# Optimization experiments

Measured on AMD Instinct MI355X. Metric: run time of the kernel, lower is better.

## Reference

```python
import jax, jax.numpy as jnp
import numpy as np

N_NODES = 100000
N_EDGES = 1600000
IN_CH = 128
HID = 128
OUT_CH = 16
N_GRAPHS = 64


def setup_inputs() -> dict:
    key = jax.random.key(0)
    ks = jax.random.split(key, 8)
    x = jax.random.normal(ks[0], (N_NODES, IN_CH), dtype=jnp.float32)
    edge_index = jax.random.randint(ks[1], (2, N_EDGES), 0, N_NODES, dtype=jnp.int64)
    batch = jnp.sort(jax.random.randint(ks[2], (N_NODES,), 0, N_GRAPHS, dtype=jnp.int64))
    s1 = 1.0 / np.sqrt(IN_CH)
    s2 = 1.0 / np.sqrt(HID)
    W1 = jax.random.uniform(ks[3], (IN_CH, HID), jnp.float32, -s1, s1)
    b1 = jnp.zeros((HID,), jnp.float32)
    W2 = jax.random.uniform(ks[4], (HID, HID), jnp.float32, -s2, s2)
    b2 = jnp.zeros((HID,), jnp.float32)
    Wfc = jax.random.uniform(ks[5], (HID, OUT_CH), jnp.float32, -s2, s2)
    bfc = jax.random.uniform(ks[6], (OUT_CH,), jnp.float32, -s2, s2)
    return {"x": x, "W1": W1, "b1": b1, "W2": W2, "b2": b2,
            "Wfc": Wfc, "bfc": bfc, "edge_index": edge_index, "batch": batch}


def _gcn_conv(x, W, b, src, dst, deg_inv_sqrt, deg_inv):
    # GCNConv with self-loops: out = D^-1/2 (A+I) D^-1/2 (x W) + b
    h = x @ W                                   # [N, H]
    norm = deg_inv_sqrt[src] * deg_inv_sqrt[dst]  # [E]
    agg = jax.ops.segment_sum(h[src] * norm[:, None], dst, num_segments=N_NODES)
    # self-loop term: deg_inv_sqrt[i]^2 * h[i]
    return agg + h * deg_inv[:, None] + b


def reference(x, W1, b1, W2, b2, Wfc, bfc, edge_index, batch):
    src, dst = edge_index[0], edge_index[1]
    # degree including self-loop
    deg = jax.ops.segment_sum(jnp.ones((N_EDGES,), jnp.float32), dst, num_segments=N_NODES) + 1.0
    deg_inv_sqrt = jax.lax.rsqrt(deg)
    deg_inv = 1.0 / deg
    h = jax.nn.relu(_gcn_conv(x, W1, b1, src, dst, deg_inv_sqrt, deg_inv))
    h = jax.nn.relu(_gcn_conv(h, W2, b2, src, dst, deg_inv_sqrt, deg_inv))
    # global mean pool over graphs
    sums = jax.ops.segment_sum(h, batch, num_segments=N_GRAPHS)          # [G, H]
    counts = jax.ops.segment_sum(jnp.ones((N_NODES,), jnp.float32), batch, num_segments=N_GRAPHS)
    pooled = sums / jnp.maximum(counts, 1.0)[:, None]
    return pooled @ Wfc + bfc
```

## Files before the change

### kernel.cpp

```cpp
#include <hip/hip_runtime.h>
#include <math.h>

#define NN 100000
#define NE 1600000
#define CH 128
#define OUTC 16
#define NG 64

#define CBSH 9
#define NCB 196
#define CHK 8192
#define MAXB 12288
#define PS 8
#define LDA 136

#define GEMMB 782
#define HISTB 196
#define PREPB 391

typedef __attribute__((ext_vector_type(8))) short bf16x8;
typedef __attribute__((ext_vector_type(4))) float f32x4;

__device__ __forceinline__ unsigned short f2bf(float f) {
    union { float f; unsigned u; } v; v.f = f;
    unsigned r = v.u + 0x7FFF + ((v.u >> 16) & 1);
    return (unsigned short)(r >> 16);
}
__device__ __forceinline__ float bflo(unsigned u) {
    union { unsigned u; float f; } v; v.u = u << 16; return v.f;
}
__device__ __forceinline__ float bfhi(unsigned u) {
    union { unsigned u; float f; } v; v.u = u & 0xffff0000u; return v.f;
}

__launch_bounds__(256, 2)
__global__ void k_fused0(const float* __restrict__ x, const float* __restrict__ W1,
                         const float* __restrict__ W2,
                         unsigned short* __restrict__ wt2,
                         const int* __restrict__ batch, int* __restrict__ gptr,
                         int* __restrict__ gfill, float* __restrict__ pooled,
                         const int* __restrict__ edst, int* __restrict__ hpart,
                         unsigned short* __restrict__ bufA) {
    __shared__ unsigned short wlds[128 * LDA];
    int b = blockIdx.x;
    int t = threadIdx.x;

    if (b < GEMMB) {
#pragma unroll
        for (int it = 0; it < 64; it++) {
            int i = it * 256 + t;
            int k = i >> 7, n = i & 127;
            wlds[n * LDA + k] = f2bf(W1[i]);
        }
        __syncthreads();

        int wave = t >> 6, lane = t & 63;
        int quad = lane >> 4, l16 = lane & 15;
        int rbase = b * 128 + wave * 32;

        bf16x8 af[2][4];
#pragma unroll
        for (int s = 0; s < 2; s++) {
            int row = rbase + s * 16 + l16;
            if (row >= NN) row = NN - 1;
            const float* arow = x + (size_t)row * CH + quad * 8;
#pragma unroll
            for (int ks = 0; ks < 4; ks++) {
                float4 lo = *(const float4*)(arow + ks * 32);
                float4 hi = *(const float4*)(arow + ks * 32 + 4);
                union { bf16x8 v; unsigned short u[8]; } tmp;
                tmp.u[0] = f2bf(lo.x); tmp.u[1] = f2bf(lo.y);
                tmp.u[2] = f2bf(lo.z); tmp.u[3] = f2bf(lo.w);
                tmp.u[4] = f2bf(hi.x); tmp.u[5] = f2bf(hi.y);
                tmp.u[6] = f2bf(hi.z); tmp.u[7] = f2bf(hi.w);
                af[s][ks] = tmp.v;
            }
        }

        f32x4 acc[2][8];
#pragma unroll
        for (int s = 0; s < 2; s++)
#pragma unroll
            for (int tt = 0; tt < 8; tt++) acc[s][tt] = (f32x4){0.f, 0.f, 0.f, 0.f};

#pragma unroll
        for (int tt = 0; tt < 8; tt++) {
            const unsigned short* wcol = &wlds[(tt * 16 + l16) * LDA + quad * 8];
            bf16x8 b0 = *(const bf16x8*)(wcol);
            bf16x8 b1 = *(const bf16x8*)(wcol + 32);
            bf16x8 b2 = *(const bf16x8*)(wcol + 64);
            bf16x8 b3 = *(const bf16x8*)(wcol + 96);
#pragma unroll
            for (int s = 0; s < 2; s++) {
                acc[s][tt] = __builtin_amdgcn_mfma_f32_16x16x32_bf16(af[s][0], b0, acc[s][tt], 0, 0, 0);
                acc[s][tt] = __builtin_amdgcn_mfma_f32_16x16x32_bf16(af[s][1], b1, acc[s][tt], 0, 0, 0);
                acc[s][tt] = __builtin_amdgcn_mfma_f32_16x16x32_bf16(af[s][2], b2, acc[s][tt], 0, 0, 0);
                acc[s][tt] = __builtin_amdgcn_mfma_f32_16x16x32_bf16(af[s][3], b3, acc[s][tt], 0, 0, 0);
            }
        }

#pragma unroll
        for (int s = 0; s < 2; s++) {
#pragma unroll
            for (int r = 0; r < 4; r++) {
                int orow = rbase + s * 16 + quad * 4 + r;
                if (orow < NN) {
#pragma unroll
                    for (int tt = 0; tt < 8; tt++)
                        bufA[(size_t)orow * CH + tt * 16 + l16] = f2bf(acc[s][tt][r]);
                }
            }
        }
    } else if (b < GEMMB + HISTB) {
        int* h = (int*)wlds;
        if (t < NCB) h[t] = 0;
        __syncthreads();
        int hb = b - GEMMB;
        int base = hb * CHK;
#pragma unroll
        for (int i = 0; i < 32; i++) {
            int e = base + i * 256 + t;
            if (e < NE) atomicAdd(&h[edst[e] >> CBSH], 1);
        }
        __syncthreads();
        if (t < NCB) hpart[hb * NCB + t] = h[t];
    } else {
        int i = (b - GEMMB - HISTB) * 256 + t;
        if (i < CH * CH) {
            int k = i >> 7, n = i & 127;
            wt2[n * CH + k] = f2bf(W2[i]);
        }
        if (i < NCB) gfill[i] = 0;
        if (i < NG * CH) pooled[i] = 0.f;
        if (i < NN) {
            int bb = batch[i];
            int prev = (i == 0) ? -1 : batch[i - 1];
            for (int g = prev + 1; g <= bb; g++) gptr[g] = i;
            if (i == NN - 1) {
                for (int g = bb + 1; g <= NG; g++) gptr[g] = NN;
            }
        }
    }
}

__global__ __launch_bounds__(256) void k_bscan(const int* __restrict__ hpart,
                                               int* __restrict__ ebase) {
    __shared__ int s[256];
    int t = threadIdx.x;
    int sum = 0;
    if (t < NCB)
        for (int b = 0; b < HISTB; b++) sum += hpart[b * NCB + t];
    s[t] = (t < NCB) ? sum : 0;
    __syncthreads();
    for (int off = 1; off < 256; off <<= 1) {
        int v = 0;
        if (t >= off) v = s[t - off];
        __syncthreads();
        s[t] += v;
        __syncthreads();
    }
    if (t == 0) ebase[0] = 0;
    if (t < NCB) ebase[t + 1] = s[t];
}

__global__ __launch_bounds__(1024) void k_passA(const int* __restrict__ src, const int* __restrict__ dst,
                        const int* __restrict__ ebase, int* __restrict__ gfill,
                        unsigned* __restrict__ ebuf) {
    __shared__ unsigned lbuf[CHK];
    __shared__ unsigned char lbyte[CHK];
    __shared__ int hcnt[NCB];
    __shared__ int hbase[256];
    __shared__ int goff[NCB];
    int t = threadIdx.x;
    if (t < NCB) hcnt[t] = 0;
    __syncthreads();
    int base = blockIdx.x * CHK;
    int cb[8], slot[8]; unsigned pk[8];
#pragma unroll
    for (int i = 0; i < 8; i++) {
        int e = base + i * 1024 + t;
        cb[i] = -1;
        if (e < NE) {
            int d = dst[e], s = src[e];
            cb[i] = d >> CBSH;
            pk[i] = ((unsigned)s << CBSH) | (unsigned)(d & 511);
            slot[i] = atomicAdd(&hcnt[cb[i]], 1);
        }
    }
    __syncthreads();
    if (t < 256) hbase[t] = (t < NCB) ? hcnt[t] : 0;
    __syncthreads();
    for (int off = 1; off < 256; off <<= 1) {
        int v = 0;
        if (t < 256 && t >= off) v = hbase[t - off];
        __syncthreads();
        if (t < 256) hbase[t] += v;
        __syncthreads();
    }
    if (t < NCB) {
        int c = hcnt[t];
        int g = c ? atomicAdd(&gfill[t], c) : 0;
        goff[t] = ebase[t] + g - (hbase[t] - c);
    }
    __syncthreads();
#pragma unroll
    for (int i = 0; i < 8; i++) {
        if (cb[i] >= 0) {
            int pos = hbase[cb[i]] - hcnt[cb[i]] + slot[i];
            lbuf[pos] = pk[i];
            lbyte[pos] = (unsigned char)cb[i];
        }
    }
    __syncthreads();
    int total = min(NE - base, CHK);
    for (int p = t; p < total; p += 1024) {
        unsigned v = lbuf[p];
        int b = lbyte[p];
        ebuf[goff[b] + p] = v;
    }
}

__global__ __launch_bounds__(1024) void k_passB(const unsigned* __restrict__ ebuf, const int* __restrict__ ebase,
                        int* __restrict__ degi, int* __restrict__ rowst,
                        float* __restrict__ dis, int* __restrict__ csr) {
    __shared__ int cnt[512];
    __shared__ int nbase[512];
    __shared__ int fill[512];
    __shared__ int stage[MAXB];
    int t = threadIdx.x;
    int cb = blockIdx.x;
    int nb0 = cb << CBSH;
    int ncnt = min(512, NN - nb0);
    int e0 = ebase[cb], e1 = ebase[cb + 1];
    if (t < 512) { cnt[t] = 0; fill[t] = 0; }
    __syncthreads();
    for (int e = e0 + t; e < e1; e += 1024)
        atomicAdd(&cnt[ebuf[e] & 511], 1);
    __syncthreads();
    if (t < 512) nbase[t] = cnt[t];
    __syncthreads();
    for (int off = 1; off < 512; off <<= 1) {
        int v = 0;
        if (t < 512 && t >= off) v = nbase[t - off];
        __syncthreads();
        if (t < 512) nbase[t] += v;
        __syncthreads();
    }
    for (int e = e0 + t; e < e1; e += 1024) {
        unsigned v = ebuf[e];
        int local = v & 511;
        int s = atomicAdd(&fill[local], 1);
        stage[nbase[local] - cnt[local] + s] = (int)(v >> CBSH);
    }
    __syncthreads();
    int total = e1 - e0;
    for (int p = t; p < total; p += 1024) csr[e0 + p] = stage[p];
    if (t < ncnt) {
        int c = cnt[t];
        degi[nb0 + t] = c;
        rowst[nb0 + t] = e0 + nbase[t] - c;
        dis[nb0 + t] = rsqrtf((float)c + 1.0f);
    }
}

__global__ __launch_bounds__(256) void k_agg_w(const unsigned short* __restrict__ ht, const int* __restrict__ rowst,
                      const int* __restrict__ degi, const int* __restrict__ csr,
                      const float* __restrict__ dis, const float* __restrict__ bias,
                      unsigned short* __restrict__ out) {
    int t = threadIdx.x;
    int grp = t >> 4;
    int q = t & 15;
    int n = blockIdx.x * 16 + grp;
    const uint4* base = (const uint4*)ht;

    float d = dis[n];
    uint4 sv = base[(size_t)n * 16 + q];
    float a[8];
    a[0] = d * bflo(sv.x); a[1] = d * bfhi(sv.x);
    a[2] = d * bflo(sv.y); a[3] = d * bfhi(sv.y);
    a[4] = d * bflo(sv.z); a[5] = d * bfhi(sv.z);
    a[6] = d * bflo(sv.w); a[7] = d * bfhi(sv.w);

    int start = rowst[n];
    int c = degi[n];
    int nb = c & ~7;
    int j = 0;
    for (; j < nb; j += 8) {
        int idx[8];
#pragma unroll
        for (int u = 0; u < 8; u++) idx[u] = csr[start + j + u];
        uint4 v[8]; float w[8];
#pragma unroll
        for (int u = 0; u < 8; u++) v[u] = base[(size_t)idx[u] * 16 + q];
#pragma unroll
        for (int u = 0; u < 8; u++) w[u] = dis[idx[u]];
#pragma unroll
        for (int u = 0; u < 8; u++) {
            a[0] = fmaf(w[u], bflo(v[u].x), a[0]); a[1] = fmaf(w[u], bfhi(v[u].x), a[1]);
            a[2] = fmaf(w[u], bflo(v[u].y), a[2]); a[3] = fmaf(w[u], bfhi(v[u].y), a[3]);
            a[4] = fmaf(w[u], bflo(v[u].z), a[4]); a[5] = fmaf(w[u], bfhi(v[u].z), a[5]);
            a[6] = fmaf(w[u], bflo(v[u].w), a[6]); a[7] = fmaf(w[u], bfhi(v[u].w), a[7]);
        }
    }
    if (j < c) {
        int idx[8];
#pragma unroll
        for (int u = 0; u < 8; u++) { int e = j + u; idx[u] = csr[start + (e < c ? e : c - 1)]; }
        uint4 v[8]; float w[8];
#pragma unroll
        for (int u = 0; u < 8; u++) v[u] = base[(size_t)idx[u] * 16 + q];
#pragma unroll
        for (int u = 0; u < 8; u++) w[u] = dis[idx[u]];
#pragma unroll
        for (int u = 0; u < 8; u++) {
            if (j + u < c) {
                a[0] = fmaf(w[u], bflo(v[u].x), a[0]); a[1] = fmaf(w[u], bfhi(v[u].x), a[1]);
                a[2] = fmaf(w[u], bflo(v[u].y), a[2]); a[3] = fmaf(w[u], bfhi(v[u].y), a[3]);
                a[4] = fmaf(w[u], bflo(v[u].z), a[4]); a[5] = fmaf(w[u], bfhi(v[u].z), a[5]);
                a[6] = fmaf(w[u], bflo(v[u].w), a[6]); a[7] = fmaf(w[u], bfhi(v[u].w), a[7]);
            }
        }
    }

    const float4* bp = (const float4*)bias;
    float4 b0 = bp[q * 2], b1 = bp[q * 2 + 1];
    uint4 o;
    {
        float ox = fmaxf(fmaf(d, a[0], b0.x), 0.f), oy = fmaxf(fmaf(d, a[1], b0.y), 0.f);
        o.x = ((unsigned)f2bf(oy) << 16) | (unsigned)f2bf(ox);
        ox = fmaxf(fmaf(d, a[2], b0.z), 0.f); oy = fmaxf(fmaf(d, a[3], b0.w), 0.f);
        o.y = ((unsigned)f2bf(oy) << 16) | (unsigned)f2bf(ox);
        ox = fmaxf(fmaf(d, a[4], b1.x), 0.f); oy = fmaxf(fmaf(d, a[5], b1.y), 0.f);
        o.z = ((unsigned)f2bf(oy) << 16) | (unsigned)f2bf(ox);
        ox = fmaxf(fmaf(d, a[6], b1.z), 0.f); oy = fmaxf(fmaf(d, a[7], b1.w), 0.f);
        o.w = ((unsigned)f2bf(oy) << 16) | (unsigned)f2bf(ox);
    }
    ((uint4*)out)[(size_t)n * 16 + q] = o;
}

__launch_bounds__(256, 2)
__global__ void k_gemm2(const unsigned short* __restrict__ Av,
                        const unsigned short* __restrict__ WT,
                        const float* __restrict__ dis,
                        unsigned short* __restrict__ out) {
    int tid = threadIdx.x;
    int wave = tid >> 6, lane = tid & 63;
    int quad = lane >> 4, l16 = lane & 15;

    int rbase = blockIdx.x * 128 + wave * 32;

    bf16x8 af[2][4];
#pragma unroll
    for (int s = 0; s < 2; s++) {
        int row = rbase + s * 16 + l16;
        if (row >= NN) row = NN - 1;
        const unsigned short* arow = Av + (size_t)row * CH + quad * 8;
#pragma unroll
        for (int ks = 0; ks < 4; ks++) af[s][ks] = *(const bf16x8*)(arow + ks * 32);
    }

    f32x4 acc[2][8];
#pragma unroll
    for (int s = 0; s < 2; s++)
#pragma unroll
        for (int t = 0; t < 8; t++) acc[s][t] = (f32x4){0.f, 0.f, 0.f, 0.f};

#pragma unroll
    for (int t = 0; t < 8; t++) {
        const unsigned short* wcol = WT + (size_t)(t * 16 + l16) * CH + quad * 8;
        bf16x8 b0 = *(const bf16x8*)(wcol);
        bf16x8 b1 = *(const bf16x8*)(wcol + 32);
        bf16x8 b2 = *(const bf16x8*)(wcol + 64);
        bf16x8 b3 = *(const bf16x8*)(wcol + 96);
#pragma unroll
        for (int s = 0; s < 2; s++) {
            acc[s][t] = __builtin_amdgcn_mfma_f32_16x16x32_bf16(af[s][0], b0, acc[s][t], 0, 0, 0);
            acc[s][t] = __builtin_amdgcn_mfma_f32_16x16x32_bf16(af[s][1], b1, acc[s][t], 0, 0, 0);
            acc[s][t] = __builtin_amdgcn_mfma_f32_16x16x32_bf16(af[s][2], b2, acc[s][t], 0, 0, 0);
            acc[s][t] = __builtin_amdgcn_mfma_f32_16x16x32_bf16(af[s][3], b3, acc[s][t], 0, 0, 0);
        }
    }

#pragma unroll
    for (int s = 0; s < 2; s++) {
#pragma unroll
        for (int r = 0; r < 4; r++) {
            int orow = rbase + s * 16 + quad * 4 + r;
            if (orow < NN) {
                float d = dis[orow];
#pragma unroll
                for (int t = 0; t < 8; t++) {
                    out[(size_t)orow * CH + t * 16 + l16] = f2bf(acc[s][t][r] * d);
                }
            }
        }
    }
}

__global__ __launch_bounds__(256) void k_agg(const unsigned short* __restrict__ ht, const int* __restrict__ rowst,
                      const int* __restrict__ degi, const int* __restrict__ csr,
                      const float* __restrict__ dis, const float* __restrict__ bias,
                      unsigned short* __restrict__ out) {
    int t = threadIdx.x;
    int grp = t >> 4;
    int q = t & 15;
    int n = blockIdx.x * 16 + grp;
    const uint4* base = (const uint4*)ht;

    uint4 sv = base[(size_t)n * 16 + q];
    float a[8];
    a[0] = bflo(sv.x); a[1] = bfhi(sv.x);
    a[2] = bflo(sv.y); a[3] = bfhi(sv.y);
    a[4] = bflo(sv.z); a[5] = bfhi(sv.z);
    a[6] = bflo(sv.w); a[7] = bfhi(sv.w);

    int start = rowst[n];
    int c = degi[n];
    int nb = c & ~7;
    int j = 0;
    for (; j < nb; j += 8) {
        int idx[8];
#pragma unroll
        for (int u = 0; u < 8; u++) idx[u] = csr[start + j + u];
        uint4 v[8];
#pragma unroll
        for (int u = 0; u < 8; u++) v[u] = base[(size_t)idx[u] * 16 + q];
#pragma unroll
        for (int u = 0; u < 8; u++) {
            a[0] += bflo(v[u].x); a[1] += bfhi(v[u].x);
            a[2] += bflo(v[u].y); a[3] += bfhi(v[u].y);
            a[4] += bflo(v[u].z); a[5] += bfhi(v[u].z);
            a[6] += bflo(v[u].w); a[7] += bfhi(v[u].w);
        }
    }
    if (j < c) {
        int idx[8];
#pragma unroll
        for (int u = 0; u < 8; u++) { int e = j + u; idx[u] = csr[start + (e < c ? e : c - 1)]; }
        uint4 v[8];
#pragma unroll
        for (int u = 0; u < 8; u++) v[u] = base[(size_t)idx[u] * 16 + q];
#pragma unroll
        for (int u = 0; u < 8; u++) {
            if (j + u < c) {
                a[0] += bflo(v[u].x); a[1] += bfhi(v[u].x);
                a[2] += bflo(v[u].y); a[3] += bfhi(v[u].y);
                a[4] += bflo(v[u].z); a[5] += bfhi(v[u].z);
                a[6] += bflo(v[u].w); a[7] += bfhi(v[u].w);
            }
        }
    }

    float d = dis[n];
    const float4* bp = (const float4*)bias;
    float4 b0 = bp[q * 2], b1 = bp[q * 2 + 1];
    uint4 o;
    {
        float ox = fmaxf(fmaf(d, a[0], b0.x), 0.f), oy = fmaxf(fmaf(d, a[1], b0.y), 0.f);
        o.x = ((unsigned)f2bf(oy) << 16) | (unsigned)f2bf(ox);
        ox = fmaxf(fmaf(d, a[2], b0.z), 0.f); oy = fmaxf(fmaf(d, a[3], b0.w), 0.f);
        o.y = ((unsigned)f2bf(oy) << 16) | (unsigned)f2bf(ox);
        ox = fmaxf(fmaf(d, a[4], b1.x), 0.f); oy = fmaxf(fmaf(d, a[5], b1.y), 0.f);
        o.z = ((unsigned)f2bf(oy) << 16) | (unsigned)f2bf(ox);
        ox = fmaxf(fmaf(d, a[6], b1.z), 0.f); oy = fmaxf(fmaf(d, a[7], b1.w), 0.f);
        o.w = ((unsigned)f2bf(oy) << 16) | (unsigned)f2bf(ox);
    }
    ((uint4*)out)[(size_t)n * 16 + q] = o;
}

__global__ __launch_bounds__(512) void k_pool2(const unsigned short* __restrict__ h,
                                               const int* __restrict__ gptr,
                                               float* __restrict__ pooled) {
    int g = blockIdx.x >> 3;
    int s = blockIdx.x & 7;
    int gs = gptr[g], ge = gptr[g + 1];
    int len = ge - gs;
    int i0 = gs + (int)(((long long)len * s) >> 3);
    int i1 = gs + (int)(((long long)len * (s + 1)) >> 3);
    int t = threadIdx.x;
    int pr = t & 63;
    int ro = t >> 6;
    const unsigned* base = (const unsigned*)h;
    float s0 = 0.f, s1 = 0.f;
    for (int n = i0 + ro; n < i1; n += 8) {
        unsigned v = base[(size_t)n * 64 + pr];
        s0 += bflo(v); s1 += bfhi(v);
    }
    __shared__ float red[2][8][64];
    red[0][ro][pr] = s0; red[1][ro][pr] = s1;
    __syncthreads();
    for (int off = 4; off >= 1; off >>= 1) {
        if (ro < off) {
            red[0][ro][pr] += red[0][ro + off][pr];
            red[1][ro][pr] += red[1][ro + off][pr];
        }
        __syncthreads();
    }
    if (ro == 0) {
        atomicAdd(&pooled[g * CH + pr * 2],     red[0][0][pr]);
        atomicAdd(&pooled[g * CH + pr * 2 + 1], red[1][0][pr]);
    }
}

__global__ void k_final(const float* __restrict__ pooled, const int* __restrict__ gptr,
                        const float* __restrict__ Wfc, const float* __restrict__ bfc,
                        float* __restrict__ out) {
    int idx = blockIdx.x * 256 + threadIdx.x;
    if (idx >= NG * OUTC) return;
    int g = idx >> 4, o = idx & 15;
    float c = (float)(gptr[g + 1] - gptr[g]);
    float inv = 1.0f / fmaxf(c, 1.0f);
    float s = 0.f;
    for (int k = 0; k < CH; k++) s += pooled[g * CH + k] * Wfc[k * OUTC + o];
    out[idx] = fmaf(s, inv, bfc[o]);
}

extern "C" void kernel_launch(void* const* d_in, const int* in_sizes, int n_in,
                              void* d_out, int out_size, void* d_ws, size_t ws_size,
                              hipStream_t stream) {
    (void)in_sizes; (void)n_in; (void)out_size; (void)ws_size;
    const float* x   = (const float*)d_in[0];
    const float* W1  = (const float*)d_in[1];
    const float* b1  = (const float*)d_in[2];
    const float* W2  = (const float*)d_in[3];
    const float* b2  = (const float*)d_in[4];
    const float* Wfc = (const float*)d_in[5];
    const float* bfc = (const float*)d_in[6];
    const int* ei    = (const int*)d_in[7];
    const int* batch = (const int*)d_in[8];
    const int* esrc = ei;
    const int* edst = ei + NE;
    float* out = (float*)d_out;

    char* w = (char*)d_ws;
    unsigned short* bufA = (unsigned short*)w; w += (size_t)NN * CH * 2;
    unsigned short* bufB = (unsigned short*)w; w += (size_t)NN * CH * 2;
    unsigned short* wt2  = (unsigned short*)w; w += (size_t)CH * CH * 2;
    unsigned* ebuf = (unsigned*)w; w += (size_t)NE * 4;
    int* csr    = (int*)w;    w += (size_t)NE * 4;
    int* degi   = (int*)w;    w += (size_t)NN * 4;
    int* rowst  = (int*)w;    w += (size_t)NN * 4;
    float* dis  = (float*)w;  w += (size_t)NN * 4;
    int* hpart  = (int*)w;    w += (size_t)HISTB * NCB * 4;
    int* ebase  = (int*)w;    w += (NCB + 1) * 4;
    int* gfill  = (int*)w;    w += NCB * 4;
    int* gptr   = (int*)w;    w += (NG + 1) * 4;
    float* pooled = (float*)w; w += (size_t)NG * CH * 4;

    const int fusedBlocks = GEMMB + HISTB + PREPB;
    const int gemmBlocks = (NN + 127) / 128;
    const int aggBlocks  = NN / 16;

    k_fused0<<<fusedBlocks, 256, 0, stream>>>(x, W1, W2, wt2, batch, gptr, gfill,
                                              pooled, edst, hpart, bufA);
    k_bscan<<<1, 256, 0, stream>>>(hpart, ebase);
    k_passA<<<HISTB, 1024, 0, stream>>>(esrc, edst, ebase, gfill, ebuf);
    k_passB<<<NCB, 1024, 0, stream>>>(ebuf, ebase, degi, rowst, dis, csr);

    k_agg_w<<<aggBlocks, 256, 0, stream>>>(bufA, rowst, degi, csr, dis, b1, bufB);
    k_gemm2<<<gemmBlocks, 256, 0, stream>>>(bufB, wt2, dis, bufA);
    k_agg<<<aggBlocks, 256, 0, stream>>>(bufA, rowst, degi, csr, dis, b2, bufB);

    k_pool2<<<NG * PS, 512, 0, stream>>>(bufB, gptr, pooled);
    k_final<<<(NG * OUTC + 255) / 256, 256, 0, stream>>>(pooled, gptr, Wfc, bfc, out);
}
```

Measured before the change: 313.7 us.

## Restructure CSR build: finer buckets, fuse scan into passA, co-schedule GEMM1 with passB

Halves the destination bucket width (256 nodes, 391 buckets) and removes the separate bucket-scan kernel. The histogram is now reduced with global atomics into a single count array, and every passA block redoes the exclusive scan itself. The first-layer GEMM moves from the early fused kernel into a new kernel alongside the per-bucket CSR finalisation, so the two overlap, and passA uses 512-thread blocks. This removes one launch and the serial hpart reduction, at the cost of redundant scans, a memset, global atomics, and LDS usage that can limit occupancy.

New measurement: 312.9 us (median of 2 runs). About the same (-0.3%).

```diff
diff --git a/kernel.cpp b/kernel.cpp
--- a/kernel.cpp
+++ b/kernel.cpp
@@ -7,16 +7,15 @@
 #define OUTC 16
 #define NG 64
 
-#define CBSH 9
-#define NCB 196
-#define CHK 8192
-#define MAXB 12288
+#define CBSH 8
+#define NCB 391
+#define CHK 4096
+#define HCHK 8192
+#define HISTB 196
+#define PREPB 391
+#define MAXB 6144
 #define PS 8
 #define LDA 136
-
-#define GEMMB 782
-#define HISTB 196
-#define PREPB 391
 
 typedef __attribute__((ext_vector_type(8))) short bf16x8;
 typedef __attribute__((ext_vector_type(4))) float f32x4;
@@ -33,19 +32,158 @@
     union { unsigned u; float f; } v; v.u = u & 0xffff0000u; return v.f;
 }
 
-__launch_bounds__(256, 2)
-__global__ void k_fused0(const float* __restrict__ x, const float* __restrict__ W1,
-                         const float* __restrict__ W2,
-                         unsigned short* __restrict__ wt2,
+__global__ __launch_bounds__(256) void k_fused0(const int* __restrict__ edst, int* __restrict__ bcnt,
+                         const float* __restrict__ W2, unsigned short* __restrict__ wt2,
                          const int* __restrict__ batch, int* __restrict__ gptr,
-                         int* __restrict__ gfill, float* __restrict__ pooled,
-                         const int* __restrict__ edst, int* __restrict__ hpart,
-                         unsigned short* __restrict__ bufA) {
-    __shared__ unsigned short wlds[128 * LDA];
+                         int* __restrict__ gfill, float* __restrict__ pooled) {
     int b = blockIdx.x;
     int t = threadIdx.x;
-
-    if (b < GEMMB) {
+    if (b < HISTB) {
+        __shared__ int h[NCB];
+        for (int i = t; i < NCB; i += 256) h[i] = 0;
+        __syncthreads();
+        int base = b * HCHK;
+#pragma unroll
+        for (int i = 0; i < 32; i++) {
+            int e = base + i * 256 + t;
+            if (e < NE) atomicAdd(&h[edst[e] >> CBSH], 1);
+        }
+        __syncthreads();
+        for (int i = t; i < NCB; i += 256)
+            if (h[i]) atomicAdd(&bcnt[i], h[i]);
+    } else {
+        int i = (b - HISTB) * 256 + t;
+        if (i < CH * CH) {
+            int k = i >> 7, n = i & 127;
+            wt2[n * CH + k] = f2bf(W2[i]);
+        }
+        if (i < NCB) gfill[i] = 0;
+        if (i < NG * CH) pooled[i] = 0.f;
+        if (i < NN) {
+            int bb = batch[i];
+            int prev = (i == 0) ? -1 : batch[i - 1];
+            for (int g = prev + 1; g <= bb; g++) gptr[g] = i;
+            if (i == NN - 1) {
+                for (int g = bb + 1; g <= NG; g++) gptr[g] = NN;
+            }
+        }
+    }
+}
+
+__global__ __launch_bounds__(512) void k_passA(const int* __restrict__ src, const int* __restrict__ dst,
+                        const int* __restrict__ bcnt, int* __restrict__ gfill,
+                        unsigned* __restrict__ ebuf, int* __restrict__ ebase) {
+    __shared__ unsigned lbuf[CHK];
+    __shared__ unsigned short lbkt[CHK];
+    __shared__ int hcnt[NCB];
+    __shared__ int hbase[512];
+    __shared__ int eb[512];
+    __shared__ int goff[NCB];
+    int t = threadIdx.x;
+    for (int i = t; i < NCB; i += 512) hcnt[i] = 0;
+    eb[t] = (t < NCB) ? bcnt[t] : 0;
+    __syncthreads();
+    int base = blockIdx.x * CHK;
+    int cb[8], slot[8]; unsigned pk[8];
+#pragma unroll
+    for (int i = 0; i < 8; i++) {
+        int e = base + i * 512 + t;
+        cb[i] = -1;
+        if (e < NE) {
+            int d = dst[e], s = src[e];
+            cb[i] = d >> CBSH;
+            pk[i] = ((unsigned)s << CBSH) | (unsigned)(d & 255);
+            slot[i] = atomicAdd(&hcnt[cb[i]], 1);
+        }
+    }
+    __syncthreads();
+    hbase[t] = (t < NCB) ? hcnt[t] : 0;
+    __syncthreads();
+    for (int off = 1; off < 512; off <<= 1) {
+        int v1 = 0, v2 = 0;
+        if (t >= off) { v1 = hbase[t - off]; v2 = eb[t - off]; }
+        __syncthreads();
+        if (t >= off) { hbase[t] += v1; eb[t] += v2; }
+        __syncthreads();
+    }
+    if (t < NCB) {
+        int c = hcnt[t];
+        int g = c ? atomicAdd(&gfill[t], c) : 0;
+        int eb_ex = t ? eb[t - 1] : 0;
+        goff[t] = eb_ex + g - (hbase[t] - c);
+    }
+    if (blockIdx.x == 0) {
+        if (t == 0) ebase[0] = 0;
+        if (t < NCB) ebase[t + 1] = eb[t];
+    }
+    __syncthreads();
+#pragma unroll
+    for (int i = 0; i < 8; i++) {
+        if (cb[i] >= 0) {
+            int pos = hbase[cb[i]] - hcnt[cb[i]] + slot[i];
+            lbuf[pos] = pk[i];
+            lbkt[pos] = (unsigned short)cb[i];
+        }
+    }
+    __syncthreads();
+    int total = min(NE - base, CHK);
+    for (int p = t; p < total; p += 512) {
+        unsigned v = lbuf[p];
+        int bk = lbkt[p];
+        ebuf[goff[bk] + p] = v;
+    }
+}
+
+__launch_bounds__(256, 2)
+__global__ void k_fusedB(const unsigned* __restrict__ ebuf, const int* __restrict__ ebase,
+                         int* __restrict__ degi, int* __restrict__ rowst,
+                         float* __restrict__ dis, int* __restrict__ csr,
+                         const float* __restrict__ x, const float* __restrict__ W1,
+                         unsigned short* __restrict__ bufA) {
+    __shared__ __align__(16) unsigned short smem[128 * LDA];
+    int b = blockIdx.x;
+    int t = threadIdx.x;
+
+    if (b < NCB) {
+        int* cnt   = (int*)smem;
+        int* nbase = cnt + 256;
+        int* fill  = nbase + 256;
+        int* stage = fill + 256;
+        int cb = b;
+        int nb0 = cb << CBSH;
+        int ncnt = min(256, NN - nb0);
+        int e0 = ebase[cb], e1 = ebase[cb + 1];
+        cnt[t] = 0; fill[t] = 0;
+        __syncthreads();
+        for (int e = e0 + t; e < e1; e += 256)
+            atomicAdd(&cnt[ebuf[e] & 255], 1);
+        __syncthreads();
+        nbase[t] = cnt[t];
+        __syncthreads();
+        for (int off = 1; off < 256; off <<= 1) {
+            int v = 0;
+            if (t >= off) v = nbase[t - off];
+            __syncthreads();
+            if (t >= off) nbase[t] += v;
+            __syncthreads();
+        }
+        for (int e = e0 + t; e < e1; e += 256) {
+            unsigned v = ebuf[e];
+            int local = v & 255;
+            int s = atomicAdd(&fill[local], 1);
+            stage[nbase[local] - cnt[local] + s] = (int)(v >> CBSH);
+        }
+        __syncthreads();
+        int total = e1 - e0;
+        for (int p = t; p < total; p += 256) csr[e0 + p] = stage[p];
+        if (t < ncnt) {
+            int c = cnt[t];
+            degi[nb0 + t] = c;
+            rowst[nb0 + t] = e0 + nbase[t] - c;
+            dis[nb0 + t] = rsqrtf((float)c + 1.0f);
+        }
+    } else {
+        unsigned short* wlds = smem;
 #pragma unroll
         for (int it = 0; it < 64; it++) {
             int i = it * 256 + t;
@@ -56,7 +194,7 @@
 
         int wave = t >> 6, lane = t & 63;
         int quad = lane >> 4, l16 = lane & 15;
-        int rbase = b * 128 + wave * 32;
+        int rbase = (b - NCB) * 128 + wave * 32;
 
         bf16x8 af[2][4];
 #pragma unroll
@@ -111,155 +249,6 @@
                 }
             }
         }
-    } else if (b < GEMMB + HISTB) {
-        int* h = (int*)wlds;
-        if (t < NCB) h[t] = 0;
-        __syncthreads();
-        int hb = b - GEMMB;
-        int base = hb * CHK;
-#pragma unroll
-        for (int i = 0; i < 32; i++) {
-            int e = base + i * 256 + t;
-            if (e < NE) atomicAdd(&h[edst[e] >> CBSH], 1);
-        }
-        __syncthreads();
-        if (t < NCB) hpart[hb * NCB + t] = h[t];
-    } else {
-        int i = (b - GEMMB - HISTB) * 256 + t;
-        if (i < CH * CH) {
-            int k = i >> 7, n = i & 127;
-            wt2[n * CH + k] = f2bf(W2[i]);
-        }
-        if (i < NCB) gfill[i] = 0;
-        if (i < NG * CH) pooled[i] = 0.f;
-        if (i < NN) {
-            int bb = batch[i];
-            int prev = (i == 0) ? -1 : batch[i - 1];
-            for (int g = prev + 1; g <= bb; g++) gptr[g] = i;
-            if (i == NN - 1) {
-                for (int g = bb + 1; g <= NG; g++) gptr[g] = NN;
-            }
-        }
-    }
-}
-
-__global__ __launch_bounds__(256) void k_bscan(const int* __restrict__ hpart,
-                                               int* __restrict__ ebase) {
-    __shared__ int s[256];
-    int t = threadIdx.x;
-    int sum = 0;
-    if (t < NCB)
-        for (int b = 0; b < HISTB; b++) sum += hpart[b * NCB + t];
-    s[t] = (t < NCB) ? sum : 0;
-    __syncthreads();
-    for (int off = 1; off < 256; off <<= 1) {
-        int v = 0;
-        if (t >= off) v = s[t - off];
-        __syncthreads();
-        s[t] += v;
-        __syncthreads();
-    }
-    if (t == 0) ebase[0] = 0;
-    if (t < NCB) ebase[t + 1] = s[t];
-}
-
-__global__ __launch_bounds__(1024) void k_passA(const int* __restrict__ src, const int* __restrict__ dst,
-                        const int* __restrict__ ebase, int* __restrict__ gfill,
-                        unsigned* __restrict__ ebuf) {
-    __shared__ unsigned lbuf[CHK];
-    __shared__ unsigned char lbyte[CHK];
-    __shared__ int hcnt[NCB];
-    __shared__ int hbase[256];
-    __shared__ int goff[NCB];
-    int t = threadIdx.x;
-    if (t < NCB) hcnt[t] = 0;
-    __syncthreads();
-    int base = blockIdx.x * CHK;
-    int cb[8], slot[8]; unsigned pk[8];
-#pragma unroll
-    for (int i = 0; i < 8; i++) {
-        int e = base + i * 1024 + t;
-        cb[i] = -1;
-        if (e < NE) {
-            int d = dst[e], s = src[e];
-            cb[i] = d >> CBSH;
-            pk[i] = ((unsigned)s << CBSH) | (unsigned)(d & 511);
-            slot[i] = atomicAdd(&hcnt[cb[i]], 1);
-        }
-    }
-    __syncthreads();
-    if (t < 256) hbase[t] = (t < NCB) ? hcnt[t] : 0;
-    __syncthreads();
-    for (int off = 1; off < 256; off <<= 1) {
-        int v = 0;
-        if (t < 256 && t >= off) v = hbase[t - off];
-        __syncthreads();
-        if (t < 256) hbase[t] += v;
-        __syncthreads();
-    }
-    if (t < NCB) {
-        int c = hcnt[t];
-        int g = c ? atomicAdd(&gfill[t], c) : 0;
-        goff[t] = ebase[t] + g - (hbase[t] - c);
-    }
-    __syncthreads();
-#pragma unroll
-    for (int i = 0; i < 8; i++) {
-        if (cb[i] >= 0) {
-            int pos = hbase[cb[i]] - hcnt[cb[i]] + slot[i];
-            lbuf[pos] = pk[i];
-            lbyte[pos] = (unsigned char)cb[i];
-        }
-    }
-    __syncthreads();
-    int total = min(NE - base, CHK);
-    for (int p = t; p < total; p += 1024) {
-        unsigned v = lbuf[p];
-        int b = lbyte[p];
-        ebuf[goff[b] + p] = v;
-    }
-}
-
-__global__ __launch_bounds__(1024) void k_passB(const unsigned* __restrict__ ebuf, const int* __restrict__ ebase,
-                        int* __restrict__ degi, int* __restrict__ rowst,
-                        float* __restrict__ dis, int* __restrict__ csr) {
-    __shared__ int cnt[512];
-    __shared__ int nbase[512];
-    __shared__ int fill[512];
-    __shared__ int stage[MAXB];
-    int t = threadIdx.x;
-    int cb = blockIdx.x;
-    int nb0 = cb << CBSH;
-    int ncnt = min(512, NN - nb0);
-    int e0 = ebase[cb], e1 = ebase[cb + 1];
-    if (t < 512) { cnt[t] = 0; fill[t] = 0; }
-    __syncthreads();
-    for (int e = e0 + t; e < e1; e += 1024)
-        atomicAdd(&cnt[ebuf[e] & 511], 1);
-    __syncthreads();
-    if (t < 512) nbase[t] = cnt[t];
-    __syncthreads();
-    for (int off = 1; off < 512; off <<= 1) {
-        int v = 0;
-        if (t < 512 && t >= off) v = nbase[t - off];
-        __syncthreads();
-        if (t < 512) nbase[t] += v;
-        __syncthreads();
-    }
-    for (int e = e0 + t; e < e1; e += 1024) {
-        unsigned v = ebuf[e];
-        int local = v & 511;
-        int s = atomicAdd(&fill[local], 1);
-        stage[nbase[local] - cnt[local] + s] = (int)(v >> CBSH);
-    }
-    __syncthreads();
-    int total = e1 - e0;
-    for (int p = t; p < total; p += 1024) csr[e0 + p] = stage[p];
-    if (t < ncnt) {
-        int c = cnt[t];
-        degi[nb0 + t] = c;
-        rowst[nb0 + t] = e0 + nbase[t] - c;
-        dis[nb0 + t] = rsqrtf((float)c + 1.0f);
     }
 }
 
@@ -541,21 +530,21 @@
     int* degi   = (int*)w;    w += (size_t)NN * 4;
     int* rowst  = (int*)w;    w += (size_t)NN * 4;
     float* dis  = (float*)w;  w += (size_t)NN * 4;
-    int* hpart  = (int*)w;    w += (size_t)HISTB * NCB * 4;
+    int* bcnt   = (int*)w;    w += NCB * 4;
     int* ebase  = (int*)w;    w += (NCB + 1) * 4;
     int* gfill  = (int*)w;    w += NCB * 4;
     int* gptr   = (int*)w;    w += (NG + 1) * 4;
     float* pooled = (float*)w; w += (size_t)NG * CH * 4;
 
-    const int fusedBlocks = GEMMB + HISTB + PREPB;
     const int gemmBlocks = (NN + 127) / 128;
     const int aggBlocks  = NN / 16;
-
-    k_fused0<<<fusedBlocks, 256, 0, stream>>>(x, W1, W2, wt2, batch, gptr, gfill,
-                                              pooled, edst, hpart, bufA);
-    k_bscan<<<1, 256, 0, stream>>>(hpart, ebase);
-    k_passA<<<HISTB, 1024, 0, stream>>>(esrc, edst, ebase, gfill, ebuf);
-    k_passB<<<NCB, 1024, 0, stream>>>(ebuf, ebase, degi, rowst, dis, csr);
+    const int passABlocks = (NE + CHK - 1) / CHK;
+
+    hipMemsetAsync(bcnt, 0, NCB * sizeof(int), stream);
+
+    k_fused0<<<HISTB + PREPB, 256, 0, stream>>>(edst, bcnt, W2, wt2, batch, gptr, gfill, pooled);
+    k_passA<<<passABlocks, 512, 0, stream>>>(esrc, edst, bcnt, gfill, ebuf, ebase);
+    k_fusedB<<<NCB + gemmBlocks, 256, 0, stream>>>(ebuf, ebase, degi, rowst, dis, csr, x, W1, bufA);
 
     k_agg_w<<<aggBlocks, 256, 0, stream>>>(bufA, rowst, degi, csr, dis, b1, bufB);
     k_gemm2<<<gemmBlocks, 256, 0, stream>>>(bufB, wt2, dis, bufA);
```
